# Optimization experiments

Measured on AMD Instinct MI355X. Metric: run time of the kernel, lower is better.

The kernel has to match this reference:

```python
import jax, jax.numpy as jnp
import numpy as np

B_J0 = 0.01
BETA = 1.8   # isAdapt=1
LENS = 0.5
DT = 1.0
IN_SIZE = 1
STRIDE = IN_SIZE
T = 784 // STRIDE
HID = (512, 512, 512)
OUT = 10
N = 256


def _create_general_mask(dim, c_min, c_max, min_dc, max_dc, phase_max, T):
    # faithful port of ASRNN_general.create_general_mask (numpy, static)
    dcs = np.linspace(min_dc, max_dc, dim)
    cycles = np.linspace(c_min, c_max, dim)
    shifts = np.linspace(0.0, float(int(phase_max * c_max)), dim)
    rows = []
    for cyc, dc, ps in zip(cycles, dcs, shifts):
        cyc = int(np.round(cyc))
        on = int(np.round(dc * cyc))
        pat = [1.0] * on + [0.0] * (cyc - on)
        ps = int(np.round(ps))
        if ps > 0:
            pat = pat[-ps:] + pat[:-ps]
        rows.append(pat * (T // cyc) + pat[: T % cyc])
    return np.asarray(rows, dtype=np.float32)  # [dim, T]

MASK1 = jnp.asarray(_create_general_mask(HID[0], 2, 8, 0.2, 0.8, 0.5, T))
MASK2 = jnp.asarray(_create_general_mask(HID[1], 4, 16, 0.2, 0.8, 0.5, T))
MASK3 = jnp.asarray(_create_general_mask(HID[2], 8, 32, 0.2, 0.8, 0.5, T))

# per-step input gather indices (faithful to the start_idx branch in forward)
_starts = np.arange(T) * STRIDE
_IDX = np.where(_starts[:, None] < T - IN_SIZE,
                _starts[:, None] + np.arange(IN_SIZE)[None, :],
                (784 - IN_SIZE) + np.arange(IN_SIZE)[None, :])  # [T, IN]


@jax.custom_vjp
def act_fun(x):
    return (x > 0.0).astype(x.dtype)

def _act_fwd(x):
    return (x > 0.0).astype(x.dtype), x

def _act_bwd(x, g):
    return (g * (jnp.abs(x) < LENS).astype(g.dtype),)

act_fun.defvjp(_act_fwd, _act_bwd)


def _mem_update(inputs, mem, spike, tau_adp, b, tau_m, mask_t):
    alpha = jnp.exp(-DT / tau_m)
    ro = jnp.exp(-DT / tau_adp)
    b_new = ro * b + (1.0 - ro) * spike
    Bth = B_J0 + BETA * b_new
    mem_new = mem * alpha + (1.0 - alpha) * inputs - Bth * spike * DT
    mem_new = jnp.where(mask_t == 0.0, mem, mem_new)
    spike_new = act_fun(mem_new - Bth) * mask_t
    return mem_new, spike_new, b_new


def _forward(x, wi1, bi1, wh1, bh1, wi2, bi2, wh2, bh2, wi3, bi3, wo, bo,
             tau_adp1, tau_adp2, tau_adp3, tau_m1, tau_m2, tau_m3):
    n = x.shape[0]
    x_seq = jnp.transpose(x[:, _IDX], (1, 0, 2))            # [T, N, IN]
    pre1 = jnp.einsum('tni,hi->tnh', x_seq, wi1) + bi1       # [T, N, H1]

    def step_fn(carry, xs):
        mem1, spk1, b1, mem2, spk2, b2, mem3, spk3, b3, out_sum, s1, s2, s3 = carry
        p1, m1, m2, m3 = xs
        h1_in = p1 + spk1 @ wh1.T + bh1
        mem1, spk1, b1 = _mem_update(h1_in, mem1, spk1, tau_adp1, b1, tau_m1, m1)
        h2_in = spk1 @ wi2.T + bi2 + spk2 @ wh2.T + bh2
        mem2, spk2, b2 = _mem_update(h2_in, mem2, spk2, tau_adp2, b2, tau_m2, m2)
        h3_in = spk2 @ wi3.T + bi3
        mem3, spk3, b3 = _mem_update(h3_in, mem3, spk3, tau_adp3, b3, tau_m3, m3)
        out_sum = out_sum + spk3 @ wo.T + bo
        return (mem1, spk1, b1, mem2, spk2, b2, mem3, spk3, b3,
                out_sum, s1 + spk1, s2 + spk2, s3 + spk3), None

    z = lambda h: jnp.zeros((n, h), x.dtype)
    f = lambda h: jnp.full((n, h), B_J0, x.dtype)
    carry0 = (z(HID[0]), z(HID[0]), f(HID[0]),
              z(HID[1]), z(HID[1]), f(HID[1]),
              z(HID[2]), z(HID[2]), f(HID[2]),
              jnp.zeros((n, OUT), x.dtype), z(HID[0]), z(HID[1]), z(HID[2]))
    xs = (pre1, MASK1.T, MASK2.T, MASK3.T)
    carry, _ = jax.lax.scan(step_fn, carry0, xs)
    out_sum, s1, s2, s3 = carry[9], carry[10], carry[11], carry[12]
    outputs = out_sum / T
    layer_fr = jnp.stack([s1.sum() / (n * HID[0] * T),
                          s2.sum() / (n * HID[1] * T),
                          s3.sum() / (n * HID[2] * T)])
    return outputs, s1 / T, s2 / T, s3 / T, layer_fr


def setup_inputs() -> dict:
    key = jax.random.key(0)
    ks = jax.random.split(key, 20)
    def xav(k, shp):
        fan_in, fan_out = shp[1], shp[0]
        s = np.sqrt(2.0 / (fan_in + fan_out))
        return jax.random.normal(k, shp, jnp.float32) * s
    return {
        'x': jax.random.uniform(ks[0], (N, 784), jnp.float32),
        'wi1': xav(ks[1], (HID[0], IN_SIZE)), 'bi1': jnp.zeros((HID[0],), jnp.float32),
        'wh1': xav(ks[2], (HID[0], HID[0])), 'bh1': jnp.zeros((HID[0],), jnp.float32),
        'wi2': xav(ks[3], (HID[1], HID[0])), 'bi2': jnp.zeros((HID[1],), jnp.float32),
        'wh2': xav(ks[4], (HID[1], HID[1])), 'bh2': jnp.zeros((HID[1],), jnp.float32),
        'wi3': xav(ks[5], (HID[2], HID[1])), 'bi3': jnp.zeros((HID[2],), jnp.float32),
        'wo': xav(ks[6], (OUT, HID[2])), 'bo': jnp.zeros((OUT,), jnp.float32),
        'tau_adp1': 700.0 + 25.0 * jax.random.normal(ks[7], (HID[0],), jnp.float32),
        'tau_adp2': 700.0 + 25.0 * jax.random.normal(ks[8], (HID[1],), jnp.float32),
        'tau_adp3': 700.0 + 25.0 * jax.random.normal(ks[9], (HID[2],), jnp.float32),
        'tau_m1': 5.0 + jax.random.normal(ks[10], (HID[0],), jnp.float32),
        'tau_m2': 5.0 + jax.random.normal(ks[11], (HID[1],), jnp.float32),
        'tau_m3': 5.0 + jax.random.normal(ks[12], (HID[2],), jnp.float32),
    }


def reference(x, wi1, bi1, wh1, bh1, wi2, bi2, wh2, bh2, wi3, bi3, wo, bo,
              tau_adp1, tau_adp2, tau_adp3, tau_m1, tau_m2, tau_m3):
    return _forward(x, wi1, bi1, wh1, bh1, wi2, bi2, wh2, bh2, wi3, bi3, wo, bo,
                    tau_adp1, tau_adp2, tau_adp3, tau_m1, tau_m2, tau_m3)
```

## Files before the change

kernel.cpp:

```cpp
#include <hip/hip_runtime.h>
#include <stdint.h>

#pragma clang fp contract(off)


static constexpr int    TS      = 784;
static constexpr size_t WS_WT1  = 0;
static constexpr size_t WS_WT2A = 1u << 20;
static constexpr size_t WS_WT2B = 2u << 20;
static constexpr size_t WS_WT3  = 3u << 20;
static constexpr size_t WS_M1   = 4u << 20;
static constexpr size_t WS_M2   = WS_M1 + (size_t)TS * 512;
static constexpr size_t WS_M3   = WS_M2 + (size_t)TS * 512;
static constexpr size_t WS_FRP  = WS_M3 + (size_t)TS * 512;

__device__ __forceinline__ float exp_np(float x) {
  float q = rintf(x * 1.442695040f);
  float r = __fmaf_rn(-q, 0.693359375f, x);
  r = __fmaf_rn(-q, -2.12194440e-4f, r);
  float r2 = r * r;
  float p = 1.9875691500e-4f;
  p = __fmaf_rn(p, r, 1.3981999507e-3f);
  p = __fmaf_rn(p, r, 8.3334519073e-3f);
  p = __fmaf_rn(p, r, 4.1665795894e-2f);
  p = __fmaf_rn(p, r, 1.6666665459e-1f);
  p = __fmaf_rn(p, r, 5.0000001201e-1f);
  p = __fmaf_rn(p, r2, r);
  p = p + 1.0f;
  return ldexpf(p, (int)q);
}

__device__ __forceinline__ int mask_val(int l, int h, int t) {
  const double cmin = (l == 0) ? 2.0 : ((l == 1) ? 4.0 : 8.0);
  const double cmax = (l == 0) ? 8.0 : ((l == 1) ? 16.0 : 32.0);
  const double smax = (l == 0) ? 4.0 : ((l == 1) ? 8.0 : 16.0);
  const double cD = (cmax - cmin) / 511.0;
  const double dD = (0.8 - 0.2) / 511.0;
  const double sD = smax / 511.0;
  const double hd = (double)h;
  double cycd = (h == 511) ? cmax : __dadd_rn(cmin, __dmul_rn(hd, cD));
  double dcd  = (h == 511) ? 0.8  : __dadd_rn(0.2,  __dmul_rn(hd, dD));
  double psd  = (h == 511) ? smax : __dmul_rn(hd, sD);
  int cyc = __double2int_rn(cycd);
  int on  = __double2int_rn(__dmul_rn(dcd, (double)cyc));
  int ps  = __double2int_rn(psd);
  int eff = (ps >= cyc) ? 0 : ps;
  int pos = (t % cyc) - eff;
  if (pos < 0) pos += cyc;
  return (pos < on) ? 1 : 0;
}

__global__ void setup_masks(char* __restrict__ ws) {
  const int t = blockIdx.x, tid = threadIdx.x;
  uint8_t* m1 = (uint8_t*)(ws + WS_M1);
  uint8_t* m2 = (uint8_t*)(ws + WS_M2);
  uint8_t* m3 = (uint8_t*)(ws + WS_M3);
  for (int h = tid; h < 512; h += 256) {
    m1[t * 512 + h] = (uint8_t)mask_val(0, h, t);
    m2[t * 512 + h] = (uint8_t)mask_val(1, h, t);
    m3[t * 512 + h] = (uint8_t)mask_val(2, h, t);
  }
}

__global__ void transpose_kernel(const float* __restrict__ wh1,
                                 const float* __restrict__ wi2,
                                 const float* __restrict__ wh2,
                                 const float* __restrict__ wi3,
                                 char* __restrict__ ws) {
  const int k = blockIdx.x;
  const int m = blockIdx.y;
  const float* W = (m == 0) ? wh1 : (m == 1) ? wi2 : (m == 2) ? wh2 : wi3;
  float* T = (float*)(ws + (size_t)m * (1u << 20));
  for (int j = threadIdx.x; j < 512; j += 256)
    T[(size_t)k * 512 + j] = W[(size_t)j * 512 + k];
}

__device__ __forceinline__ uint32_t upd32(float hin, uint32_t mk, uint32_t osp,
                                          float al, float om, float r, float omr,
                                          float& memv, float& bv) {
  float t1 = r * bv;
  float bn = osp ? (t1 + omr) : t1;
  float bt = 1.8f * bn;
  float Bth = 0.01f + bt;
  float m1 = memv * al;
  float m2 = om * hin;
  float m3 = m1 + m2;
  float mn = osp ? (m3 - Bth) : m3;
  if (!mk) mn = memv;
  uint32_t sn = (mk && (mn - Bth) > 0.0f) ? 1u : 0u;
  memv = mn; bv = bn;
  return sn;
}

__device__ __forceinline__ int expand_list(const uint64_t* __restrict__ bm,
                                           uint32_t mysp, int h,
                                           ushort* __restrict__ kl) {
  const int wh = h >> 6, bpos = h & 63;
  int cnt = 0, rank = 0;
#pragma unroll
  for (int w = 0; w < 8; ++w) {
    uint64_t v = bm[w];
    int pc = __builtin_popcountll(v);
    if (w < wh) rank += pc;
    cnt += pc;
  }
  rank += __builtin_popcountll(bm[wh] & ((1ull << bpos) - 1ull));
  if (mysp) kl[rank] = (ushort)h;
  return cnt;
}

__device__ __forceinline__ float gather_from(const float* __restrict__ base,
                                             const ushort* kl, int from, int cnt,
                                             float s) {
  int i = from;
  for (; i + 16 <= cnt; i += 16) {
    float w0  = base[(size_t)kl[i + 0]  << 9];
    float w1  = base[(size_t)kl[i + 1]  << 9];
    float w2  = base[(size_t)kl[i + 2]  << 9];
    float w3  = base[(size_t)kl[i + 3]  << 9];
    float w4  = base[(size_t)kl[i + 4]  << 9];
    float w5  = base[(size_t)kl[i + 5]  << 9];
    float w6  = base[(size_t)kl[i + 6]  << 9];
    float w7  = base[(size_t)kl[i + 7]  << 9];
    float w8  = base[(size_t)kl[i + 8]  << 9];
    float w9  = base[(size_t)kl[i + 9]  << 9];
    float w10 = base[(size_t)kl[i + 10] << 9];
    float w11 = base[(size_t)kl[i + 11] << 9];
    float w12 = base[(size_t)kl[i + 12] << 9];
    float w13 = base[(size_t)kl[i + 13] << 9];
    float w14 = base[(size_t)kl[i + 14] << 9];
    float w15 = base[(size_t)kl[i + 15] << 9];
    s = s + w0;  s = s + w1;  s = s + w2;  s = s + w3;
    s = s + w4;  s = s + w5;  s = s + w6;  s = s + w7;
    s = s + w8;  s = s + w9;  s = s + w10; s = s + w11;
    s = s + w12; s = s + w13; s = s + w14; s = s + w15;
  }
  for (; i + 4 <= cnt; i += 4) {
    float w0 = base[(size_t)kl[i + 0] << 9];
    float w1 = base[(size_t)kl[i + 1] << 9];
    float w2 = base[(size_t)kl[i + 2] << 9];
    float w3 = base[(size_t)kl[i + 3] << 9];
    s = s + w0; s = s + w1; s = s + w2; s = s + w3;
  }
  for (; i < cnt; ++i) s = s + base[(size_t)kl[i] << 9];
  return s;
}

__device__ __forceinline__ void dual_gather(
    const float* __restrict__ bA, const ushort* __restrict__ klA, int cntA,
    const float* __restrict__ bB, const ushort* __restrict__ klB, int cntB,
    float& outA, float& outB) {
  float a = 0.0f, b = 0.0f;
  int iA = 0, iB = 0;
  while (iA + 8 <= cntA && iB + 8 <= cntB) {
    float wa0 = bA[(size_t)klA[iA + 0] << 9];
    float wa1 = bA[(size_t)klA[iA + 1] << 9];
    float wa2 = bA[(size_t)klA[iA + 2] << 9];
    float wa3 = bA[(size_t)klA[iA + 3] << 9];
    float wa4 = bA[(size_t)klA[iA + 4] << 9];
    float wa5 = bA[(size_t)klA[iA + 5] << 9];
    float wa6 = bA[(size_t)klA[iA + 6] << 9];
    float wa7 = bA[(size_t)klA[iA + 7] << 9];
    float wb0 = bB[(size_t)klB[iB + 0] << 9];
    float wb1 = bB[(size_t)klB[iB + 1] << 9];
    float wb2 = bB[(size_t)klB[iB + 2] << 9];
    float wb3 = bB[(size_t)klB[iB + 3] << 9];
    float wb4 = bB[(size_t)klB[iB + 4] << 9];
    float wb5 = bB[(size_t)klB[iB + 5] << 9];
    float wb6 = bB[(size_t)klB[iB + 6] << 9];
    float wb7 = bB[(size_t)klB[iB + 7] << 9];
    a = a + wa0; a = a + wa1; a = a + wa2; a = a + wa3;
    a = a + wa4; a = a + wa5; a = a + wa6; a = a + wa7;
    b = b + wb0; b = b + wb1; b = b + wb2; b = b + wb3;
    b = b + wb4; b = b + wb5; b = b + wb6; b = b + wb7;
    iA += 8; iB += 8;
  }
  a = gather_from(bA, klA, iA, cntA, a);
  b = gather_from(bB, klB, iB, cntB, b);
  outA = a; outB = b;
}

__global__ __launch_bounds__(512, 1) void rnn_block(
    const float* __restrict__ x,
    const float* __restrict__ wi1, const float* __restrict__ bi1,
    const float* __restrict__ bh1,
    const float* __restrict__ bi2, const float* __restrict__ bh2,
    const float* __restrict__ bi3,
    const float* __restrict__ wo, const float* __restrict__ bo,
    const float* __restrict__ ta1, const float* __restrict__ ta2,
    const float* __restrict__ ta3, const float* __restrict__ tm1,
    const float* __restrict__ tm2, const float* __restrict__ tm3,
    char* __restrict__ ws, float* __restrict__ d_out) {
  const int n = blockIdx.x;
  const int h = threadIdx.x;
  const float* WT1  = (const float*)(ws + WS_WT1);
  const float* WT2A = (const float*)(ws + WS_WT2A);
  const float* WT2B = (const float*)(ws + WS_WT2B);
  const float* WT3  = (const float*)(ws + WS_WT3);
  const uint8_t* M1 = (const uint8_t*)(ws + WS_M1);
  const uint8_t* M2 = (const uint8_t*)(ws + WS_M2);
  const uint8_t* M3 = (const uint8_t*)(ws + WS_M3);

  __shared__ uint64_t bm1s[8], bm2s[8], bm3s[8];
  __shared__ ushort kl1s[512], kl2s[512];
  __shared__ float woS[10 * 513];
  __shared__ double red[512];

  for (int i = h; i < 5120; i += 512) woS[(i / 512) * 513 + (i % 512)] = wo[i];

  float al1 = exp_np(-1.0f / tm1[h]), om1 = 1.0f - al1;
  float ro1 = exp_np(-1.0f / ta1[h]), omr1 = 1.0f - ro1;
  float al2 = exp_np(-1.0f / tm2[h]), om2 = 1.0f - al2;
  float ro2 = exp_np(-1.0f / ta2[h]), omr2 = 1.0f - ro2;
  float al3 = exp_np(-1.0f / tm3[h]), om3 = 1.0f - al3;
  float ro3 = exp_np(-1.0f / ta3[h]), omr3 = 1.0f - ro3;
  float wi1v = wi1[h], bi1v = bi1[h], bh1v = bh1[h];
  float bi2v = bi2[h], bh2v = bh2[h], bi3v = bi3[h];
  float bo_v = (h < 80 && (h & 7) == 0) ? bo[h >> 3] : 0.0f;

  float mem1 = 0.0f, b1 = 0.01f, c1 = 0.0f;
  float mem2 = 0.0f, b2 = 0.01f, c2 = 0.0f;
  float mem3 = 0.0f, b3 = 0.01f, c3 = 0.0f;
  uint32_t sp1 = 0, sp2 = 0, sp3 = 0;
  int cnt1 = 0, cnt2 = 0;
  float outv = 0.0f;
  float acc1 = 0.0f;
  uint32_t mk1 = M1[h];

  const float* xrow = x + (size_t)n * 784;
  __syncthreads();

  for (int t = 0; t < TS; ++t) {
    const uint32_t mk2 = M2[t * 512 + h];
    const uint32_t mk3 = M3[t * 512 + h];
    const float xv = xrow[t];

    float p1 = xv * wi1v;
    p1 = p1 + bi1v;
    p1 = p1 + acc1;
    p1 = p1 + bh1v;
    uint32_t sn1 = upd32(p1, mk1, sp1, al1, om1, ro1, omr1, mem1, b1);
    sp1 = sn1; c1 += (float)sn1;
    uint64_t bal1 = __ballot(sn1);
    if ((h & 63) == 0) bm1s[h >> 6] = bal1;
    __syncthreads();
    cnt1 = expand_list(bm1s, sn1, h, kl1s);
    __syncthreads();

    float a1, a2;
    {
      const int cA = mk2 ? cnt1 : 0;
      const int cB = mk2 ? cnt2 : 0;
      dual_gather(WT2A + h, kl1s, cA, WT2B + h, kl2s, cB, a1, a2);
    }
    float p2 = a1 + bi2v;
    p2 = p2 + a2;
    p2 = p2 + bh2v;
    uint32_t sn2 = upd32(p2, mk2, sp2, al2, om2, ro2, omr2, mem2, b2);
    sp2 = sn2; c2 += (float)sn2;
    uint64_t bal2 = __ballot(sn2);
    if ((h & 63) == 0) bm2s[h >> 6] = bal2;
    __syncthreads();
    cnt2 = expand_list(bm2s, sn2, h, kl2s);
    __syncthreads();

    const uint32_t mk1n = (t + 1 < TS) ? M1[(t + 1) * 512 + h] : 0u;
    float a3, a1n;
    {
      const int cG3 = mk3 ? cnt2 : 0;
      const int cG1 = mk1n ? cnt1 : 0;
      dual_gather(WT3 + h, kl2s, cG3, WT1 + h, kl1s, cG1, a3, a1n);
    }
    acc1 = a1n;
    mk1 = mk1n;
    float p3 = a3 + bi3v;
    uint32_t sn3 = upd32(p3, mk3, sp3, al3, om3, ro3, omr3, mem3, b3);
    sp3 = sn3; c3 += (float)sn3;
    uint64_t bal3 = __ballot(sn3);
    if ((h & 63) == 0) bm3s[h >> 6] = bal3;
    __syncthreads();

    if (h < 80) {
      const int w = h & 7;
      uint64_t v = bm3s[w];
      float s = 0.0f;
      const float* wrow = &woS[(h >> 3) * 513 + w * 64];
      while (v) { int b = __builtin_ctzll(v); v &= v - 1; s = s + wrow[b]; }
      s += __shfl_down(s, 4, 8);
      s += __shfl_down(s, 2, 8);
      s += __shfl_down(s, 1, 8);
      if (w == 0) { float vv = outv + s; outv = vv + bo_v; }
    }
  }

  d_out[2560 + (size_t)n * 512 + h]          = c1 / 784.0f;
  d_out[2560 + 131072 + (size_t)n * 512 + h] = c2 / 784.0f;
  d_out[2560 + 262144 + (size_t)n * 512 + h] = c3 / 784.0f;
  if (h < 80 && (h & 7) == 0) d_out[(size_t)n * 10 + (h >> 3)] = outv / 784.0f;

  double* FRP = (double*)(ws + WS_FRP);
  red[h] = (double)c1;
  __syncthreads();
  for (int wd = 256; wd > 0; wd >>= 1) {
    if (h < wd) red[h] += red[h + wd];
    __syncthreads();
  }
  if (h == 0) FRP[n * 3 + 0] = red[0];
  __syncthreads();
  red[h] = (double)c2;
  __syncthreads();
  for (int wd = 256; wd > 0; wd >>= 1) {
    if (h < wd) red[h] += red[h + wd];
    __syncthreads();
  }
  if (h == 0) FRP[n * 3 + 1] = red[0];
  __syncthreads();
  red[h] = (double)c3;
  __syncthreads();
  for (int wd = 256; wd > 0; wd >>= 1) {
    if (h < wd) red[h] += red[h + wd];
    __syncthreads();
  }
  if (h == 0) FRP[n * 3 + 2] = red[0];
}

__global__ void finalize_fr(char* __restrict__ ws, float* __restrict__ d_out) {
  const int l = threadIdx.x;
  if (l >= 3) return;
  const double* FRP = (const double*)(ws + WS_FRP);
  double s = 0.0;
  for (int n = 0; n < 256; ++n) s += FRP[n * 3 + l];
  d_out[395776 + l] = (float)(s / (131072.0 * 784.0));
}

extern "C" void kernel_launch(void* const* d_in, const int* in_sizes, int n_in,
                              void* d_out, int out_size, void* d_ws, size_t ws_size,
                              hipStream_t stream) {
  (void)in_sizes; (void)n_in; (void)out_size; (void)ws_size;
  const float* x   = (const float*)d_in[0];
  const float* wi1 = (const float*)d_in[1];
  const float* bi1 = (const float*)d_in[2];
  const float* wh1 = (const float*)d_in[3];
  const float* bh1 = (const float*)d_in[4];
  const float* wi2 = (const float*)d_in[5];
  const float* bi2 = (const float*)d_in[6];
  const float* wh2 = (const float*)d_in[7];
  const float* bh2 = (const float*)d_in[8];
  const float* wi3 = (const float*)d_in[9];
  const float* bi3 = (const float*)d_in[10];
  const float* wo  = (const float*)d_in[11];
  const float* bo  = (const float*)d_in[12];
  const float* ta1 = (const float*)d_in[13];
  const float* ta2 = (const float*)d_in[14];
  const float* ta3 = (const float*)d_in[15];
  const float* tm1 = (const float*)d_in[16];
  const float* tm2 = (const float*)d_in[17];
  const float* tm3 = (const float*)d_in[18];
  char*  ws  = (char*)d_ws;
  float* out = (float*)d_out;

  hipLaunchKernelGGL(setup_masks, dim3(TS), dim3(256), 0, stream, ws);
  hipLaunchKernelGGL(transpose_kernel, dim3(512, 4), dim3(256), 0, stream,
                     wh1, wi2, wh2, wi3, ws);
  hipLaunchKernelGGL(rnn_block, dim3(256), dim3(512), 0, stream,
                     x, wi1, bi1, bh1, bi2, bh2, bi3, wo, bo,
                     ta1, ta2, ta3, tm1, tm2, tm3, ws, out);
  hipLaunchKernelGGL(finalize_fr, dim3(1), dim3(64), 0, stream, ws, out);
}
```

Baseline: 4.748 ms.

## Accumulate output layer per-thread in registers and reduce once after loop

Replaces the per-timestep ballot, barrier and serial output-weight summation with per-thread register accumulation of wo contributions whenever a layer-3 neuron spikes. A single block-wide double-precision reduction over threads runs after the time loop, and the bias is added as 784*bo. This removes one __syncthreads and a serialized bit-scan loop from each of the 784 steps. In exchange it adds 20 registers per thread and changes the floating-point summation order relative to the reference.

Result: faster. 4.301 ms (-9.4%).

```diff
diff --git a/kernel.cpp b/kernel.cpp
--- a/kernel.cpp
+++ b/kernel.cpp
@@ -201,12 +201,10 @@
   const uint8_t* M2 = (const uint8_t*)(ws + WS_M2);
   const uint8_t* M3 = (const uint8_t*)(ws + WS_M3);
 
-  __shared__ uint64_t bm1s[8], bm2s[8], bm3s[8];
+  __shared__ uint64_t bm1s[8], bm2s[8];
   __shared__ ushort kl1s[512], kl2s[512];
-  __shared__ float woS[10 * 513];
+  __shared__ float outpS[512 * 10];
   __shared__ double red[512];
-
-  for (int i = h; i < 5120; i += 512) woS[(i / 512) * 513 + (i % 512)] = wo[i];
 
   float al1 = exp_np(-1.0f / tm1[h]), om1 = 1.0f - al1;
   float ro1 = exp_np(-1.0f / ta1[h]), omr1 = 1.0f - ro1;
@@ -216,14 +214,16 @@
   float ro3 = exp_np(-1.0f / ta3[h]), omr3 = 1.0f - ro3;
   float wi1v = wi1[h], bi1v = bi1[h], bh1v = bh1[h];
   float bi2v = bi2[h], bh2v = bh2[h], bi3v = bi3[h];
-  float bo_v = (h < 80 && (h & 7) == 0) ? bo[h >> 3] : 0.0f;
+
+  float wov[10], outp[10];
+#pragma unroll
+  for (int o = 0; o < 10; ++o) { wov[o] = wo[(size_t)o * 512 + h]; outp[o] = 0.0f; }
 
   float mem1 = 0.0f, b1 = 0.01f, c1 = 0.0f;
   float mem2 = 0.0f, b2 = 0.01f, c2 = 0.0f;
   float mem3 = 0.0f, b3 = 0.01f, c3 = 0.0f;
   uint32_t sp1 = 0, sp2 = 0, sp3 = 0;
   int cnt1 = 0, cnt2 = 0;
-  float outv = 0.0f;
   float acc1 = 0.0f;
   uint32_t mk1 = M1[h];
 
@@ -276,27 +276,26 @@
     float p3 = a3 + bi3v;
     uint32_t sn3 = upd32(p3, mk3, sp3, al3, om3, ro3, omr3, mem3, b3);
     sp3 = sn3; c3 += (float)sn3;
-    uint64_t bal3 = __ballot(sn3);
-    if ((h & 63) == 0) bm3s[h >> 6] = bal3;
-    __syncthreads();
-
-    if (h < 80) {
-      const int w = h & 7;
-      uint64_t v = bm3s[w];
-      float s = 0.0f;
-      const float* wrow = &woS[(h >> 3) * 513 + w * 64];
-      while (v) { int b = __builtin_ctzll(v); v &= v - 1; s = s + wrow[b]; }
-      s += __shfl_down(s, 4, 8);
-      s += __shfl_down(s, 2, 8);
-      s += __shfl_down(s, 1, 8);
-      if (w == 0) { float vv = outv + s; outv = vv + bo_v; }
+
+    if (sn3) {
+#pragma unroll
+      for (int o = 0; o < 10; ++o) outp[o] = outp[o] + wov[o];
     }
   }
 
   d_out[2560 + (size_t)n * 512 + h]          = c1 / 784.0f;
   d_out[2560 + 131072 + (size_t)n * 512 + h] = c2 / 784.0f;
   d_out[2560 + 262144 + (size_t)n * 512 + h] = c3 / 784.0f;
-  if (h < 80 && (h & 7) == 0) d_out[(size_t)n * 10 + (h >> 3)] = outv / 784.0f;
+
+#pragma unroll
+  for (int o = 0; o < 10; ++o) outpS[h * 10 + o] = outp[o];
+  __syncthreads();
+  if (h < 10) {
+    double s = 0.0;
+    for (int l = 0; l < 512; ++l) s += (double)outpS[l * 10 + h];
+    s += 784.0 * (double)bo[h];
+    d_out[(size_t)n * 10 + h] = (float)s / 784.0f;
+  }
 
   double* FRP = (double*)(ws + WS_FRP);
   red[h] = (double)c1;
```
